# Optimization experiments

Hardware: AMD Instinct MI355X
Metric: run time of the kernel (lower is better)

The kernel has to match this reference:

```python
import jax, jax.numpy as jnp
import numpy as np

N_HEAD = 16


def setup_inputs() -> dict:
    key = jax.random.key(0)
    ks = jax.random.split(key, 5)
    B, T, C = 2, 2048, 1024
    s = 1.0 / np.sqrt(C)
    inp = {
        "x": jax.random.normal(ks[0], (B, T, C), dtype=jnp.float32),
        "Wq": jax.random.normal(ks[1], (C, C), dtype=jnp.float32) * s,
        "bq": jnp.zeros((C,), dtype=jnp.float32),
        "Wk": jax.random.normal(ks[2], (C, C), dtype=jnp.float32) * s,
        "bk": jnp.zeros((C,), dtype=jnp.float32),
        "Wv": jax.random.normal(ks[3], (C, C), dtype=jnp.float32) * s,
        "bv": jnp.zeros((C,), dtype=jnp.float32),
        "Wp": jax.random.normal(ks[4], (C, C), dtype=jnp.float32) * s,
        "bp": jnp.zeros((C,), dtype=jnp.float32),
    }
    return inp


def reference(x, Wq, bq, Wk, bk, Wv, bv, Wp, bp):
    B, T, C = x.shape
    H = N_HEAD
    D = C // H
    # linear projections (torch Linear: x @ W.T + b)
    q = (x @ Wq.T + bq).reshape(B, T, H, D)
    k = (x @ Wk.T + bk).reshape(B, T, H, D)
    v = (x @ Wv.T + bv).reshape(B, T, H, D)
    # scaled dot-product attention (NO causal mask in original forward)
    att = jnp.einsum("bthd,bshd->bhts", q, k) * (1.0 / np.sqrt(D))
    att = jax.nn.softmax(att, axis=-1)
    y = jnp.einsum("bhts,bshd->bthd", att, v).reshape(B, T, C)
    # output projection (dropouts are identity at p=0 / eval)
    return y @ Wp.T + bp
```

## Files before the change

kernel.cpp:

```cpp
#include <hip/hip_runtime.h>
#include <hip/hip_bf16.h>

typedef __attribute__((ext_vector_type(4))) float f32x4;
typedef __attribute__((ext_vector_type(16))) float f32x16;
typedef __attribute__((ext_vector_type(8))) short bf16x8;
typedef __attribute__((ext_vector_type(2))) unsigned int u32x2;

#define T_SEQ 2048
#define C_DIM 1024
#define NH 16
#define DHD 64

__device__ __forceinline__ unsigned cvtpk_bf16(float lo, float hi) {
    unsigned r;
    asm("v_cvt_pk_bf16_f32 %0, %1, %2" : "=v"(r) : "v"(lo), "v"(hi));
    return r;
}

__device__ __forceinline__ float exp2_hw(float x) {
    float r;
    asm("v_exp_f32 %0, %1" : "=v"(r) : "v"(x));
    return r;
}

__device__ __forceinline__ void async_copy16(void* lds, const void* g) {
    __builtin_amdgcn_global_load_lds(
        (const __attribute__((address_space(1))) unsigned int*)(uintptr_t)g,
        (__attribute__((address_space(3))) unsigned int*)(unsigned int)(uintptr_t)lds,
        16, 0, 0);
}

__global__ __launch_bounds__(256) void cvt_all(const float* __restrict__ x,
                                               const float* __restrict__ Wq, const float* __restrict__ Wk,
                                               const float* __restrict__ Wv, const float* __restrict__ Wp,
                                               __hip_bfloat16* __restrict__ xb,
                                               __hip_bfloat16* __restrict__ wf,
                                               __hip_bfloat16* __restrict__ wpb) {
    int i = blockIdx.x * blockDim.x + threadIdx.x;
    const float* src; __hip_bfloat16* dst; int off;
    if (i < 1048576) { src = x; dst = xb; off = i; }
    else {
        int j = i - 1048576; int wi = j >> 18; off = j & 262143;
        switch (wi) {
            case 0:  src = Wq; dst = wf;           break;
            case 1:  src = Wk; dst = wf + 1048576; break;
            case 2:  src = Wv; dst = wf + 2097152; break;
            default: src = Wp; dst = wpb;          break;
        }
    }
    float4 v = *(const float4*)(src + (size_t)off * 4);
    union { __hip_bfloat16 h[4]; u32x2 u; } p;
    p.h[0] = __float2bfloat16(v.x); p.h[1] = __float2bfloat16(v.y);
    p.h[2] = __float2bfloat16(v.z); p.h[3] = __float2bfloat16(v.w);
    *(u32x2*)(dst + (size_t)off * 4) = p.u;
}

__global__ __launch_bounds__(512) void gemm_qkv(const __hip_bfloat16* __restrict__ A,
                                                const __hip_bfloat16* __restrict__ Bw,
                                                const float* __restrict__ biasq,
                                                const float* __restrict__ biask,
                                                const float* __restrict__ biasv,
                                                __hip_bfloat16* __restrict__ oq,
                                                __hip_bfloat16* __restrict__ okk,
                                                __hip_bfloat16* __restrict__ ovt) {
    __shared__ __align__(16) char lds[131072];

    const int wg = ((int)blockIdx.x & 7) * 32 + ((int)blockIdx.x >> 3);
    const int m0 = (wg & 31) * 128;
    const int n0 = (wg >> 5) * 384;

    const int tid = threadIdx.x;
    const int w = tid >> 6, l = tid & 63;
    const int wr = w >> 2, wc = w & 3;
    const int lg = l >> 4, lr = l & 15;

    const int sr0 = tid >> 3;
    const int sc0 = (tid & 7) * 16;
    const int gc0 = sc0 ^ ((sr0 & 7) << 4);
    const size_t goff = (size_t)sr0 * 2048 + gc0;

    const char* Ag = (const char*)A + (size_t)m0 * 2048;
    const char* Bg = (const char*)Bw + (size_t)n0 * 2048;

    auto STAGE_A = [&](int buf, int half, int kt) {
        const char* g = Ag + (size_t)(half * 64) * 2048 + kt * 128 + goff;
        char* d = lds + (buf * 2 + half) * 8192 + w * 1024;
        async_copy16(d, g);
    };
    auto STAGE_B = [&](int buf, int half, int kt) {
        #pragma unroll
        for (int p = 0; p < 3; p++) {
            const char* g = Bg + (size_t)(half * 192 + p * 64) * 2048 + kt * 128 + goff;
            char* d = lds + 32768 + (buf * 2 + half) * 24576 + p * 8192 + w * 1024;
            async_copy16(d, g);
        }
    };

    const int sw = (lr & 7) << 4;
    auto LDA = [&](bf16x8* af, int buf) {
        const char* base = lds + (buf * 2 + wr) * 8192;
        #pragma unroll
        for (int m = 0; m < 4; m++) {
            const int r = m * 16 + lr;
            #pragma unroll
            for (int kk = 0; kk < 2; kk++)
                af[m * 2 + kk] = *(const bf16x8*)(base + r * 128 + ((kk * 64 + lg * 16) ^ sw));
        }
    };
    auto LDB = [&](bf16x8* bfv, int buf, int nq) {
        const char* base = lds + 32768 + (buf * 2 + (wc >> 1)) * 24576;
        #pragma unroll
        for (int n = 0; n < 2; n++) {
            const int r = (wc & 1) * 96 + (nq * 2 + n) * 16 + lr;
            #pragma unroll
            for (int kk = 0; kk < 2; kk++)
                bfv[n * 2 + kk] = *(const bf16x8*)(base + r * 128 + ((kk * 64 + lg * 16) ^ sw));
        }
    };

    f32x4 acc[4][6] = {};
    auto MF = [&](const bf16x8* af, const bf16x8* bfv, int nq) {
        #pragma unroll
        for (int m = 0; m < 4; m++)
            #pragma unroll
            for (int n = 0; n < 2; n++)
                #pragma unroll
                for (int kk = 0; kk < 2; kk++)
                    acc[m][nq * 2 + n] = __builtin_amdgcn_mfma_f32_16x16x32_bf16(
                        af[m * 2 + kk], bfv[n * 2 + kk], acc[m][nq * 2 + n], 0, 0, 0);
    };

#define PH_OPEN()  __builtin_amdgcn_sched_barrier(0); \
                   __builtin_amdgcn_s_barrier(); \
                   asm volatile("s_waitcnt lgkmcnt(0)" ::: "memory"); \
                   __builtin_amdgcn_sched_barrier(0); \
                   __builtin_amdgcn_s_setprio(1);
#define PH_CLOSE() __builtin_amdgcn_s_setprio(0); \
                   __builtin_amdgcn_sched_barrier(0); \
                   __builtin_amdgcn_s_barrier();
#define PH_CLOSE_VM2() __builtin_amdgcn_s_setprio(0); \
                   asm volatile("s_waitcnt vmcnt(2)" ::: "memory"); \
                   __builtin_amdgcn_sched_barrier(0); \
                   __builtin_amdgcn_s_barrier();
#define PH_CLOSE_VM5() __builtin_amdgcn_s_setprio(0); \
                   asm volatile("s_waitcnt vmcnt(5)" ::: "memory"); \
                   __builtin_amdgcn_sched_barrier(0); \
                   __builtin_amdgcn_s_barrier();

    bf16x8 af[8], bfA[4], bfB[4], bfC[4];

    STAGE_B(0, 0, 0); STAGE_B(0, 1, 0); STAGE_A(0, 0, 0); STAGE_A(0, 1, 0);
    STAGE_A(1, 0, 1); STAGE_A(1, 1, 1); STAGE_B(1, 0, 1);
    asm volatile("s_waitcnt vmcnt(5)" ::: "memory");
    __builtin_amdgcn_sched_barrier(0);
    __builtin_amdgcn_s_barrier();

    for (int it = 0; it < 8; ++it) {
        const int t1 = 2 * it + 1;
        const int c2 = (2 * it + 2 < 16) ? 2 * it + 2 : 14;
        const int c3 = (2 * it + 3 < 16) ? 2 * it + 3 : 15;
        const int b2 = c2 & 1, b3 = c3 & 1;

        LDA(af, 0); LDB(bfA, 0, 0);
        STAGE_B(1, 1, t1);
        PH_OPEN(); MF(af, bfA, 0); PH_CLOSE();
        LDB(bfB, 0, 1);
        STAGE_A(b2, 0, c2); STAGE_A(b2, 1, c2);
        PH_OPEN(); MF(af, bfB, 1); PH_CLOSE();
        LDB(bfC, 0, 2);
        PH_OPEN(); MF(af, bfC, 2); PH_CLOSE_VM2();

        LDA(af, 1); LDB(bfA, 1, 0);
        STAGE_B(b2, 0, c2);
        PH_OPEN(); MF(af, bfA, 0); PH_CLOSE();
        LDB(bfB, 1, 1);
        STAGE_B(b2, 1, c2); STAGE_A(b3, 0, c3); STAGE_A(b3, 1, c3);
        PH_OPEN(); MF(af, bfB, 1); PH_CLOSE();
        LDB(bfC, 1, 2);
        STAGE_B(b3, 0, c3);
        PH_OPEN(); MF(af, bfC, 2); PH_CLOSE_VM5();
    }
#undef PH_OPEN
#undef PH_CLOSE
#undef PH_CLOSE_VM2
#undef PH_CLOSE_VM5

    #pragma unroll
    for (int m = 0; m < 4; m++) {
        const int rowb = m0 + wr * 64 + m * 16 + lg * 4;
        const int b = rowb >> 11, t0r = rowb & 2047;
        #pragma unroll
        for (int nf = 0; nf < 6; nf++) {
            const int col = n0 + wc * 96 + nf * 16 + lr;
            const int proj = col >> 10;
            const int colL = col & 1023;
            const int hh = colL >> 6, dd = colL & 63;
            if (proj < 2) {
                const float* bias = (proj == 0) ? biasq : biask;
                const float bsc = (proj == 0) ? 0.125f * 1.4426950408889634f : 1.0f;
                __hip_bfloat16* dst = (proj == 0) ? oq : okk;
                #pragma unroll
                for (int rr = 0; rr < 4; rr++) {
                    const int row = rowb + rr;
                    float val = (acc[m][nf][rr] + bias[colL]) * bsc;
                    dst[(((size_t)(b * NH + hh)) * T_SEQ + (row & 2047)) * DHD + dd] = __float2bfloat16(val);
                }
            } else {
                const float bv = biasv[colL];
                union { __hip_bfloat16 h[4]; u32x2 u; } p;
                #pragma unroll
                for (int rr = 0; rr < 4; rr++)
                    p.h[rr] = __float2bfloat16(acc[m][nf][rr] + bv);
                *(u32x2*)&ovt[(((size_t)(b * NH + hh)) * DHD + dd) * T_SEQ + t0r] = p.u;
            }
        }
    }
}

__global__ __launch_bounds__(256) void gemm_proj(const __hip_bfloat16* __restrict__ A,
                                                 const __hip_bfloat16* __restrict__ Bw,
                                                 const float* __restrict__ biasp,
                                                 float* __restrict__ outf) {
    __shared__ __align__(16) char As[128 * 128];
    __shared__ __align__(16) char Bs[128 * 128];

    const int nwg = gridDim.x;
    const int cpx = nwg >> 3;
    const int wg = ((int)blockIdx.x & 7) * cpx + ((int)blockIdx.x >> 3);
    const int m0 = (wg & 31) * 128;
    const int n0 = (wg >> 5) * 128;

    const int tid = threadIdx.x;
    const int w = tid >> 6, l = tid & 63;
    const int wr = w >> 1, wc = w & 1;
    const int lg = l >> 4, lr = l & 15;

    const char* Ag = (const char*)A + (size_t)m0 * 2048;
    const char* Bg = (const char*)Bw + (size_t)n0 * 2048;
    const int lrow = l >> 3;
    const int scol = (l & 7) * 16;

    f32x4 acc[4][4] = {};

    for (int kt = 0; kt < 16; ++kt) {
        __syncthreads();
        #pragma unroll
        for (int i = 0; i < 4; i++) {
            const int rb = w * 32 + i * 8;
            const size_t go = (size_t)(rb + lrow) * 2048 + (size_t)kt * 128 + scol;
            async_copy16(&As[rb * 128], Ag + go);
            async_copy16(&Bs[rb * 128], Bg + go);
        }
        __syncthreads();
        #pragma unroll
        for (int kk = 0; kk < 2; kk++) {
            bf16x8 af[4], bfr[4];
            #pragma unroll
            for (int m = 0; m < 4; m++)
                af[m] = *(const bf16x8*)(&As[(wr * 64 + m * 16 + lr) * 128 + kk * 64 + lg * 16]);
            #pragma unroll
            for (int n = 0; n < 4; n++)
                bfr[n] = *(const bf16x8*)(&Bs[(wc * 64 + n * 16 + lr) * 128 + kk * 64 + lg * 16]);
            #pragma unroll
            for (int m = 0; m < 4; m++)
                #pragma unroll
                for (int n = 0; n < 4; n++)
                    acc[m][n] = __builtin_amdgcn_mfma_f32_16x16x32_bf16(af[m], bfr[n], acc[m][n], 0, 0, 0);
        }
    }

    #pragma unroll
    for (int m = 0; m < 4; m++)
        #pragma unroll
        for (int n = 0; n < 4; n++)
            #pragma unroll
            for (int r = 0; r < 4; r++) {
                int row = m0 + wr * 64 + m * 16 + lg * 4 + r;
                int col = n0 + wc * 64 + n * 16 + lr;
                outf[(size_t)row * C_DIM + col] = acc[m][n][r] + biasp[col];
            }
}

__global__ __launch_bounds__(256) void attn8(const __hip_bfloat16* __restrict__ Q,
                                             const __hip_bfloat16* __restrict__ K,
                                             const __hip_bfloat16* __restrict__ Vt,
                                             __hip_bfloat16* __restrict__ Y) {
    const int bid = blockIdx.x;
    const int xcd = bid & 7, slot = bid >> 3;
    const int head = xcd * 4 + (slot & 3);
    const int qblk = slot >> 2;

    const int tid = threadIdx.x;
    const int w = tid >> 6, l = tid & 63;
    const int lq = l & 31, hi = l >> 5;
    const int q0 = qblk * 128 + w * 32;

    __shared__ __align__(16) char Ks[3][8192];
    __shared__ __align__(16) char Vs[3][8192];
    __shared__ float bc[4][32];

    const char* Kb = (const char*)(K + (size_t)head * T_SEQ * DHD);
    const char* Vb = (const char*)(Vt + (size_t)head * DHD * T_SEQ);

    bf16x8 qf[4];
    {
        const char* qrow = (const char*)(Q + ((size_t)head * T_SEQ + q0 + lq) * DHD);
        #pragma unroll
        for (int t = 0; t < 4; t++) qf[t] = *(const bf16x8*)(qrow + t * 32 + hi * 16);
    }

    f32x16 yacc[2] = {};
    float ls0 = 0.f, ls1 = 0.f, ls2 = 0.f, ls3 = 0.f;

    const int o0 = (2 * w) * 1024 + l * 16;
    const int o1 = o0 + 1024;
    const int r0 = o0 >> 7, c0b = o0 & 127;
    const int r1 = o1 >> 7, c1b = o1 & 127;
    const int wads0 = r0 * 128 + (c0b ^ ((r0 & 7) << 4));
    const int wads1 = r1 * 128 + (c1b ^ ((r1 & 7) << 4));
    const char* vsrc0 = Vb + (size_t)r0 * (T_SEQ * 2) + c0b;
    const char* vsrc1 = Vb + (size_t)r1 * (T_SEQ * 2) + c1b;

    float4 kreg0, kreg1, vreg0, vreg1;
    auto stage_load = [&](int tile) {
        const char* kb2 = Kb + (size_t)tile * 8192;
        kreg0 = *(const float4*)(kb2 + o0);
        kreg1 = *(const float4*)(kb2 + o1);
        vreg0 = *(const float4*)(vsrc0 + (size_t)tile * 128);
        vreg1 = *(const float4*)(vsrc1 + (size_t)tile * 128);
    };
    auto stage_write = [&](int buf) {
        *(float4*)(&Ks[buf][wads0]) = kreg0;
        *(float4*)(&Ks[buf][wads1]) = kreg1;
        *(float4*)(&Vs[buf][wads0]) = vreg0;
        *(float4*)(&Vs[buf][wads1]) = vreg1;
    };

    auto qk = [&](int buf, f32x16& s0h, f32x16& s1h) {
        s0h = f32x16{}; s1h = f32x16{};
        const char* base0 = Ks[buf] + lq * 128;
        const char* base1 = Ks[buf] + (32 + lq) * 128;
        const int sw0 = (lq & 7) << 4;
        __builtin_amdgcn_s_setprio(1);
        #pragma unroll
        for (int t = 0; t < 4; t++) {
            bf16x8 kf0 = *(const bf16x8*)(base0 + ((t * 32 + hi * 16) ^ sw0));
            s0h = __builtin_amdgcn_mfma_f32_32x32x16_bf16(kf0, qf[t], s0h, 0, 0, 0);
        }
        #pragma unroll
        for (int t = 0; t < 4; t++) {
            bf16x8 kf1 = *(const bf16x8*)(base1 + ((t * 32 + hi * 16) ^ sw0));
            s1h = __builtin_amdgcn_mfma_f32_32x32x16_bf16(kf1, qf[t], s1h, 0, 0, 0);
        }
        __builtin_amdgcn_s_setprio(0);
    };

    auto sm_exp = [&](f32x16& a, f32x16& b) {
        #pragma unroll
        for (int r = 0; r < 16; r += 4) {
            a[r + 0] = exp2_hw(a[r + 0]); a[r + 1] = exp2_hw(a[r + 1]);
            a[r + 2] = exp2_hw(a[r + 2]); a[r + 3] = exp2_hw(a[r + 3]);
            b[r + 0] = exp2_hw(b[r + 0]); b[r + 1] = exp2_hw(b[r + 1]);
            b[r + 2] = exp2_hw(b[r + 2]); b[r + 3] = exp2_hw(b[r + 3]);
            ls0 += a[r + 0] + b[r + 0];
            ls1 += a[r + 1] + b[r + 1];
            ls2 += a[r + 2] + b[r + 2];
            ls3 += a[r + 3] + b[r + 3];
        }
    };

    auto pv = [&](int buf, const f32x16& a, const f32x16& b) {
        unsigned pw0[8], pw1[8];
        #pragma unroll
        for (int M = 0; M < 4; M++) {
            const int u = M * 4;
            pw0[M] = cvtpk_bf16(a[u + 0], a[u + 1]);
            pw1[M] = cvtpk_bf16(a[u + 2], a[u + 3]);
            pw0[M + 4] = cvtpk_bf16(b[u + 0], b[u + 1]);
            pw1[M + 4] = cvtpk_bf16(b[u + 2], b[u + 3]);
        }
        __builtin_amdgcn_s_setprio(1);
        #pragma unroll
        for (int t = 0; t < 4; t++) {
            u32x2 s0p = __builtin_amdgcn_permlane32_swap(pw0[2 * t], pw0[2 * t + 1], false, false);
            u32x2 s1p = __builtin_amdgcn_permlane32_swap(pw1[2 * t], pw1[2 * t + 1], false, false);
            union { unsigned u[4]; bf16x8 v; } af;
            af.u[0] = s0p.x; af.u[1] = s1p.x; af.u[2] = s0p.y; af.u[3] = s1p.y;
            #pragma unroll
            for (int dh = 0; dh < 2; dh++) {
                const int row = dh * 32 + lq;
                bf16x8 vf = *(const bf16x8*)(&Vs[buf][row * 128 + ((t * 32 + hi * 16) ^ ((row & 7) << 4))]);
                yacc[dh] = __builtin_amdgcn_mfma_f32_32x32x16_bf16(af.v, vf, yacc[dh], 0, 0, 0);
            }
        }
        __builtin_amdgcn_s_setprio(0);
    };

    f32x16 sA0, sA1, sB0, sB1;
    stage_load(0); stage_write(0);
    stage_load(1); stage_write(1);
    stage_load(2);
    __syncthreads();
    qk(0, sA0, sA1);

    for (int t = 0; t < 32; t += 2) {
        qk((t + 1) % 3, sB0, sB1);
        if (t + 2 < 32) {
            asm volatile("s_waitcnt vmcnt(0)" ::: "memory");
            stage_write((t + 2) % 3);
            if (t + 3 < 32) stage_load(t + 3);
        }
        sm_exp(sA0, sA1);
        pv(t % 3, sA0, sA1);
        asm volatile("s_waitcnt lgkmcnt(0)" ::: "memory");
        __builtin_amdgcn_s_barrier();
        __builtin_amdgcn_sched_barrier(0);

        const int t1 = t + 1;
        if (t1 + 1 < 32) qk((t1 + 1) % 3, sA0, sA1);
        if (t1 + 2 < 32) {
            asm volatile("s_waitcnt vmcnt(0)" ::: "memory");
            stage_write((t1 + 2) % 3);
            if (t1 + 3 < 32) stage_load(t1 + 3);
        }
        sm_exp(sB0, sB1);
        pv(t1 % 3, sB0, sB1);
        asm volatile("s_waitcnt lgkmcnt(0)" ::: "memory");
        __builtin_amdgcn_s_barrier();
        __builtin_amdgcn_sched_barrier(0);
    }

    float lsum = (ls0 + ls1) + (ls2 + ls3);
    lsum += __shfl_xor(lsum, 32);
    float inv = 1.0f / lsum;
    if (hi == 0) bc[w][lq] = inv;
    asm volatile("s_waitcnt lgkmcnt(0)" ::: "memory");
    __builtin_amdgcn_sched_barrier(0);

    const int b = head >> 4, h16 = head & 15;
    const size_t rowbase = (size_t)b * T_SEQ + q0;
    #pragma unroll
    for (int r = 0; r < 16; r++) {
        const int crow = (r & 3) + 8 * (r >> 2) + 4 * hi;
        const float iv = bc[w][crow];
        const size_t row = rowbase + crow;
        Y[row * C_DIM + h16 * DHD + lq]      = __float2bfloat16(yacc[0][r] * iv);
        Y[row * C_DIM + h16 * DHD + 32 + lq] = __float2bfloat16(yacc[1][r] * iv);
    }
}

extern "C" void kernel_launch(void* const* d_in, const int* in_sizes, int n_in,
                              void* d_out, int out_size, void* d_ws, size_t ws_size,
                              hipStream_t stream) {
    (void)in_sizes; (void)n_in; (void)out_size; (void)ws_size;
    const float* x  = (const float*)d_in[0];
    const float* Wq = (const float*)d_in[1];
    const float* bq = (const float*)d_in[2];
    const float* Wk = (const float*)d_in[3];
    const float* bk = (const float*)d_in[4];
    const float* Wv = (const float*)d_in[5];
    const float* bv = (const float*)d_in[6];
    const float* Wp = (const float*)d_in[7];
    const float* bp = (const float*)d_in[8];
    float* out = (float*)d_out;

    char* ws = (char*)d_ws;
    const size_t MC = (size_t)4096 * C_DIM;
    const size_t CC = (size_t)C_DIM * C_DIM;
    __hip_bfloat16* xb  = (__hip_bfloat16*)ws;  ws += MC * 2;
    __hip_bfloat16* wf  = (__hip_bfloat16*)ws;  ws += 3 * CC * 2;
    __hip_bfloat16* wpb = (__hip_bfloat16*)ws;  ws += CC * 2;
    __hip_bfloat16* qb  = (__hip_bfloat16*)ws;  ws += MC * 2;
    __hip_bfloat16* kb  = (__hip_bfloat16*)ws;  ws += MC * 2;
    __hip_bfloat16* vtb = (__hip_bfloat16*)ws;  ws += MC * 2;
    __hip_bfloat16* yb  = (__hip_bfloat16*)ws;  ws += MC * 2;

    cvt_all<<<8192, 256, 0, stream>>>(x, Wq, Wk, Wv, Wp, xb, wf, wpb);

    gemm_qkv<<<256, 512, 0, stream>>>(xb, wf, bq, bk, bv, qb, kb, vtb);

    attn8<<<512, 256, 0, stream>>>(qb, kb, vtb, yb);

    gemm_proj<<<256, 256, 0, stream>>>(yb, wpb, bp, out);
}
```

Baseline: 119.2 us.

## Process 64 query rows per wave in attention to reuse K/V fragments

Each attention wave now computes two 32-row query tiles against every K/V tile loaded into shared memory, doubling MFMA work per LDS fragment read and halving the grid to 256 blocks. The two-stage ping-pong of score tiles is replaced by a simple single-tile loop with a rotating triple buffer. This cuts LDS traffic and global K/V reloads per query, at the cost of more registers, fewer resident waves and less overlap between QK, softmax and PV phases.

Result: slower. 123.4 us (+3.5%).

```diff
diff --git a/kernel.cpp b/kernel.cpp
--- a/kernel.cpp
+++ b/kernel.cpp
@@ -281,10 +281,10 @@
             }
 }
 
-__global__ __launch_bounds__(256) void attn8(const __hip_bfloat16* __restrict__ Q,
-                                             const __hip_bfloat16* __restrict__ K,
-                                             const __hip_bfloat16* __restrict__ Vt,
-                                             __hip_bfloat16* __restrict__ Y) {
+__global__ __launch_bounds__(256) void attn10(const __hip_bfloat16* __restrict__ Q,
+                                              const __hip_bfloat16* __restrict__ K,
+                                              const __hip_bfloat16* __restrict__ Vt,
+                                              __hip_bfloat16* __restrict__ Y) {
     const int bid = blockIdx.x;
     const int xcd = bid & 7, slot = bid >> 3;
     const int head = xcd * 4 + (slot & 3);
@@ -293,24 +293,29 @@
     const int tid = threadIdx.x;
     const int w = tid >> 6, l = tid & 63;
     const int lq = l & 31, hi = l >> 5;
-    const int q0 = qblk * 128 + w * 32;
+    const int q0 = qblk * 256 + w * 64;
 
     __shared__ __align__(16) char Ks[3][8192];
     __shared__ __align__(16) char Vs[3][8192];
-    __shared__ float bc[4][32];
+    __shared__ float bc[4][64];
 
     const char* Kb = (const char*)(K + (size_t)head * T_SEQ * DHD);
     const char* Vb = (const char*)(Vt + (size_t)head * DHD * T_SEQ);
 
-    bf16x8 qf[4];
+    bf16x8 qfA[4], qfB[4];
     {
-        const char* qrow = (const char*)(Q + ((size_t)head * T_SEQ + q0 + lq) * DHD);
-        #pragma unroll
-        for (int t = 0; t < 4; t++) qf[t] = *(const bf16x8*)(qrow + t * 32 + hi * 16);
-    }
-
-    f32x16 yacc[2] = {};
-    float ls0 = 0.f, ls1 = 0.f, ls2 = 0.f, ls3 = 0.f;
+        const char* qrowA = (const char*)(Q + ((size_t)head * T_SEQ + q0 + lq) * DHD);
+        const char* qrowB = qrowA + 32 * DHD * 2;
+        #pragma unroll
+        for (int t = 0; t < 4; t++) {
+            qfA[t] = *(const bf16x8*)(qrowA + t * 32 + hi * 16);
+            qfB[t] = *(const bf16x8*)(qrowB + t * 32 + hi * 16);
+        }
+    }
+
+    f32x16 yacc[4] = {};
+    float lsA0 = 0.f, lsA1 = 0.f, lsA2 = 0.f, lsA3 = 0.f;
+    float lsB0 = 0.f, lsB1 = 0.f, lsB2 = 0.f, lsB3 = 0.f;
 
     const int o0 = (2 * w) * 1024 + l * 16;
     const int o1 = o0 + 1024;
@@ -336,8 +341,10 @@
         *(float4*)(&Vs[buf][wads1]) = vreg1;
     };
 
-    auto qk = [&](int buf, f32x16& s0h, f32x16& s1h) {
-        s0h = f32x16{}; s1h = f32x16{};
+    f32x16 sA0, sA1, sC0, sC1;
+
+    auto qk = [&](int buf) {
+        sA0 = f32x16{}; sA1 = f32x16{}; sC0 = f32x16{}; sC1 = f32x16{};
         const char* base0 = Ks[buf] + lq * 128;
         const char* base1 = Ks[buf] + (32 + lq) * 128;
         const int sw0 = (lq & 7) << 4;
@@ -345,107 +352,109 @@
         #pragma unroll
         for (int t = 0; t < 4; t++) {
             bf16x8 kf0 = *(const bf16x8*)(base0 + ((t * 32 + hi * 16) ^ sw0));
-            s0h = __builtin_amdgcn_mfma_f32_32x32x16_bf16(kf0, qf[t], s0h, 0, 0, 0);
+            sA0 = __builtin_amdgcn_mfma_f32_32x32x16_bf16(kf0, qfA[t], sA0, 0, 0, 0);
+            sC0 = __builtin_amdgcn_mfma_f32_32x32x16_bf16(kf0, qfB[t], sC0, 0, 0, 0);
         }
         #pragma unroll
         for (int t = 0; t < 4; t++) {
             bf16x8 kf1 = *(const bf16x8*)(base1 + ((t * 32 + hi * 16) ^ sw0));
-            s1h = __builtin_amdgcn_mfma_f32_32x32x16_bf16(kf1, qf[t], s1h, 0, 0, 0);
+            sA1 = __builtin_amdgcn_mfma_f32_32x32x16_bf16(kf1, qfA[t], sA1, 0, 0, 0);
+            sC1 = __builtin_amdgcn_mfma_f32_32x32x16_bf16(kf1, qfB[t], sC1, 0, 0, 0);
         }
         __builtin_amdgcn_s_setprio(0);
     };
 
-    auto sm_exp = [&](f32x16& a, f32x16& b) {
+    auto sm_exp = [&]() {
         #pragma unroll
         for (int r = 0; r < 16; r += 4) {
-            a[r + 0] = exp2_hw(a[r + 0]); a[r + 1] = exp2_hw(a[r + 1]);
-            a[r + 2] = exp2_hw(a[r + 2]); a[r + 3] = exp2_hw(a[r + 3]);
-            b[r + 0] = exp2_hw(b[r + 0]); b[r + 1] = exp2_hw(b[r + 1]);
-            b[r + 2] = exp2_hw(b[r + 2]); b[r + 3] = exp2_hw(b[r + 3]);
-            ls0 += a[r + 0] + b[r + 0];
-            ls1 += a[r + 1] + b[r + 1];
-            ls2 += a[r + 2] + b[r + 2];
-            ls3 += a[r + 3] + b[r + 3];
-        }
-    };
-
-    auto pv = [&](int buf, const f32x16& a, const f32x16& b) {
-        unsigned pw0[8], pw1[8];
+            sA0[r+0]=exp2_hw(sA0[r+0]); sA0[r+1]=exp2_hw(sA0[r+1]); sA0[r+2]=exp2_hw(sA0[r+2]); sA0[r+3]=exp2_hw(sA0[r+3]);
+            sA1[r+0]=exp2_hw(sA1[r+0]); sA1[r+1]=exp2_hw(sA1[r+1]); sA1[r+2]=exp2_hw(sA1[r+2]); sA1[r+3]=exp2_hw(sA1[r+3]);
+            sC0[r+0]=exp2_hw(sC0[r+0]); sC0[r+1]=exp2_hw(sC0[r+1]); sC0[r+2]=exp2_hw(sC0[r+2]); sC0[r+3]=exp2_hw(sC0[r+3]);
+            sC1[r+0]=exp2_hw(sC1[r+0]); sC1[r+1]=exp2_hw(sC1[r+1]); sC1[r+2]=exp2_hw(sC1[r+2]); sC1[r+3]=exp2_hw(sC1[r+3]);
+            lsA0 += sA0[r+0] + sA1[r+0];  lsA1 += sA0[r+1] + sA1[r+1];
+            lsA2 += sA0[r+2] + sA1[r+2];  lsA3 += sA0[r+3] + sA1[r+3];
+            lsB0 += sC0[r+0] + sC1[r+0];  lsB1 += sC0[r+1] + sC1[r+1];
+            lsB2 += sC0[r+2] + sC1[r+2];  lsB3 += sC0[r+3] + sC1[r+3];
+        }
+    };
+
+    auto pv = [&](int buf) {
+        unsigned pwA0[8], pwA1[8], pwB0[8], pwB1[8];
         #pragma unroll
         for (int M = 0; M < 4; M++) {
             const int u = M * 4;
-            pw0[M] = cvtpk_bf16(a[u + 0], a[u + 1]);
-            pw1[M] = cvtpk_bf16(a[u + 2], a[u + 3]);
-            pw0[M + 4] = cvtpk_bf16(b[u + 0], b[u + 1]);
-            pw1[M + 4] = cvtpk_bf16(b[u + 2], b[u + 3]);
+            pwA0[M]     = cvtpk_bf16(sA0[u+0], sA0[u+1]);  pwA1[M]     = cvtpk_bf16(sA0[u+2], sA0[u+3]);
+            pwA0[M + 4] = cvtpk_bf16(sA1[u+0], sA1[u+1]);  pwA1[M + 4] = cvtpk_bf16(sA1[u+2], sA1[u+3]);
+            pwB0[M]     = cvtpk_bf16(sC0[u+0], sC0[u+1]);  pwB1[M]     = cvtpk_bf16(sC0[u+2], sC0[u+3]);
+            pwB0[M + 4] = cvtpk_bf16(sC1[u+0], sC1[u+1]);  pwB1[M + 4] = cvtpk_bf16(sC1[u+2], sC1[u+3]);
         }
         __builtin_amdgcn_s_setprio(1);
         #pragma unroll
         for (int t = 0; t < 4; t++) {
-            u32x2 s0p = __builtin_amdgcn_permlane32_swap(pw0[2 * t], pw0[2 * t + 1], false, false);
-            u32x2 s1p = __builtin_amdgcn_permlane32_swap(pw1[2 * t], pw1[2 * t + 1], false, false);
-            union { unsigned u[4]; bf16x8 v; } af;
-            af.u[0] = s0p.x; af.u[1] = s1p.x; af.u[2] = s0p.y; af.u[3] = s1p.y;
+            u32x2 a0 = __builtin_amdgcn_permlane32_swap(pwA0[2*t], pwA0[2*t+1], false, false);
+            u32x2 a1 = __builtin_amdgcn_permlane32_swap(pwA1[2*t], pwA1[2*t+1], false, false);
+            u32x2 b0 = __builtin_amdgcn_permlane32_swap(pwB0[2*t], pwB0[2*t+1], false, false);
+            u32x2 b1 = __builtin_amdgcn_permlane32_swap(pwB1[2*t], pwB1[2*t+1], false, false);
+            union { unsigned u[4]; bf16x8 v; } afA, afB;
+            afA.u[0] = a0.x; afA.u[1] = a1.x; afA.u[2] = a0.y; afA.u[3] = a1.y;
+            afB.u[0] = b0.x; afB.u[1] = b1.x; afB.u[2] = b0.y; afB.u[3] = b1.y;
             #pragma unroll
             for (int dh = 0; dh < 2; dh++) {
                 const int row = dh * 32 + lq;
                 bf16x8 vf = *(const bf16x8*)(&Vs[buf][row * 128 + ((t * 32 + hi * 16) ^ ((row & 7) << 4))]);
-                yacc[dh] = __builtin_amdgcn_mfma_f32_32x32x16_bf16(af.v, vf, yacc[dh], 0, 0, 0);
+                yacc[dh]     = __builtin_amdgcn_mfma_f32_32x32x16_bf16(afA.v, vf, yacc[dh],     0, 0, 0);
+                yacc[2 + dh] = __builtin_amdgcn_mfma_f32_32x32x16_bf16(afB.v, vf, yacc[2 + dh], 0, 0, 0);
             }
         }
         __builtin_amdgcn_s_setprio(0);
     };
 
-    f32x16 sA0, sA1, sB0, sB1;
     stage_load(0); stage_write(0);
     stage_load(1); stage_write(1);
     stage_load(2);
     __syncthreads();
-    qk(0, sA0, sA1);
-
-    for (int t = 0; t < 32; t += 2) {
-        qk((t + 1) % 3, sB0, sB1);
-        if (t + 2 < 32) {
+
+    int buf = 0;
+    for (int t = 0; t < 32; ++t) {
+        qk(buf);
+        if (t < 30) {
             asm volatile("s_waitcnt vmcnt(0)" ::: "memory");
-            stage_write((t + 2) % 3);
-            if (t + 3 < 32) stage_load(t + 3);
-        }
-        sm_exp(sA0, sA1);
-        pv(t % 3, sA0, sA1);
+            int wb = buf + 2; if (wb >= 3) wb -= 3;
+            stage_write(wb);
+            if (t < 29) stage_load(t + 3);
+        }
+        sm_exp();
+        pv(buf);
         asm volatile("s_waitcnt lgkmcnt(0)" ::: "memory");
         __builtin_amdgcn_s_barrier();
         __builtin_amdgcn_sched_barrier(0);
-
-        const int t1 = t + 1;
-        if (t1 + 1 < 32) qk((t1 + 1) % 3, sA0, sA1);
-        if (t1 + 2 < 32) {
-            asm volatile("s_waitcnt vmcnt(0)" ::: "memory");
-            stage_write((t1 + 2) % 3);
-            if (t1 + 3 < 32) stage_load(t1 + 3);
-        }
-        sm_exp(sB0, sB1);
-        pv(t1 % 3, sB0, sB1);
-        asm volatile("s_waitcnt lgkmcnt(0)" ::: "memory");
-        __builtin_amdgcn_s_barrier();
-        __builtin_amdgcn_sched_barrier(0);
-    }
-
-    float lsum = (ls0 + ls1) + (ls2 + ls3);
-    lsum += __shfl_xor(lsum, 32);
-    float inv = 1.0f / lsum;
-    if (hi == 0) bc[w][lq] = inv;
+        if (++buf == 3) buf = 0;
+    }
+
+    float lsumA = (lsA0 + lsA1) + (lsA2 + lsA3);
+    float lsumB = (lsB0 + lsB1) + (lsB2 + lsB3);
+    lsumA += __shfl_xor(lsumA, 32);
+    lsumB += __shfl_xor(lsumB, 32);
+    if (hi == 0) {
+        bc[w][lq] = 1.0f / lsumA;
+        bc[w][32 + lq] = 1.0f / lsumB;
+    }
     asm volatile("s_waitcnt lgkmcnt(0)" ::: "memory");
     __builtin_amdgcn_sched_barrier(0);
 
     const int b = head >> 4, h16 = head & 15;
-    const size_t rowbase = (size_t)b * T_SEQ + q0;
+    const size_t rowbaseA = (size_t)b * T_SEQ + q0;
     #pragma unroll
     for (int r = 0; r < 16; r++) {
         const int crow = (r & 3) + 8 * (r >> 2) + 4 * hi;
-        const float iv = bc[w][crow];
-        const size_t row = rowbase + crow;
-        Y[row * C_DIM + h16 * DHD + lq]      = __float2bfloat16(yacc[0][r] * iv);
-        Y[row * C_DIM + h16 * DHD + 32 + lq] = __float2bfloat16(yacc[1][r] * iv);
+        const float ivA = bc[w][crow];
+        const float ivB = bc[w][32 + crow];
+        const size_t rowA = rowbaseA + crow;
+        const size_t rowB = rowA + 32;
+        Y[rowA * C_DIM + h16 * DHD + lq]      = __float2bfloat16(yacc[0][r] * ivA);
+        Y[rowA * C_DIM + h16 * DHD + 32 + lq] = __float2bfloat16(yacc[1][r] * ivA);
+        Y[rowB * C_DIM + h16 * DHD + lq]      = __float2bfloat16(yacc[2][r] * ivB);
+        Y[rowB * C_DIM + h16 * DHD + 32 + lq] = __float2bfloat16(yacc[3][r] * ivB);
     }
 }
 
@@ -479,7 +488,7 @@
 
     gemm_qkv<<<256, 512, 0, stream>>>(xb, wf, bq, bk, bv, qb, kb, vtb);
 
-    attn8<<<512, 256, 0, stream>>>(qb, kb, vtb, yb);
+    attn10<<<256, 256, 0, stream>>>(qb, kb, vtb, yb);
 
     gemm_proj<<<256, 256, 0, stream>>>(yb, wpb, bp, out);
 }
```

## Rewrite output projection GEMM with 8-wave double-buffered pipelined schedule

Applied to the files above, without the earlier changes.

Replaces the 4-wave output projection GEMM with a 512-thread version. The new kernel double-buffers A/B tiles in 64KB LDS with an XOR-swizzled layout to avoid bank conflicts. It interleaves async global-to-LDS copies with MFMA phases using sched barriers, setprio and partial vmcnt waits, so that load latency is hidden behind compute. The cost is more LDS per block and a fragile hand-tuned barrier schedule. This GEMM is only one of four kernels, which caps the possible overall gain.

After: 113.0 us, median of 2. 5.3% less time.

```diff
diff --git a/kernel.cpp b/kernel.cpp
--- a/kernel.cpp
+++ b/kernel.cpp
@@ -217,66 +217,122 @@
     }
 }
 
-__global__ __launch_bounds__(256) void gemm_proj(const __hip_bfloat16* __restrict__ A,
-                                                 const __hip_bfloat16* __restrict__ Bw,
-                                                 const float* __restrict__ biasp,
-                                                 float* __restrict__ outf) {
-    __shared__ __align__(16) char As[128 * 128];
-    __shared__ __align__(16) char Bs[128 * 128];
-
-    const int nwg = gridDim.x;
-    const int cpx = nwg >> 3;
-    const int wg = ((int)blockIdx.x & 7) * cpx + ((int)blockIdx.x >> 3);
+__global__ __launch_bounds__(512) void gemm_proj2(const __hip_bfloat16* __restrict__ A,
+                                                  const __hip_bfloat16* __restrict__ Bw,
+                                                  const float* __restrict__ biasp,
+                                                  float* __restrict__ outf) {
+    __shared__ __align__(16) char lds[65536];
+
+    const int wg = ((int)blockIdx.x & 7) * 32 + ((int)blockIdx.x >> 3);
     const int m0 = (wg & 31) * 128;
     const int n0 = (wg >> 5) * 128;
 
     const int tid = threadIdx.x;
     const int w = tid >> 6, l = tid & 63;
-    const int wr = w >> 1, wc = w & 1;
+    const int wr = w >> 2, wc = w & 3;
     const int lg = l >> 4, lr = l & 15;
+
+    const int sr0 = tid >> 3;
+    const int sc0 = (tid & 7) * 16;
+    const int gc0 = sc0 ^ ((sr0 & 7) << 4);
+    const size_t goff = (size_t)sr0 * 2048 + gc0;
 
     const char* Ag = (const char*)A + (size_t)m0 * 2048;
     const char* Bg = (const char*)Bw + (size_t)n0 * 2048;
-    const int lrow = l >> 3;
-    const int scol = (l & 7) * 16;
-
-    f32x4 acc[4][4] = {};
-
-    for (int kt = 0; kt < 16; ++kt) {
-        __syncthreads();
-        #pragma unroll
-        for (int i = 0; i < 4; i++) {
-            const int rb = w * 32 + i * 8;
-            const size_t go = (size_t)(rb + lrow) * 2048 + (size_t)kt * 128 + scol;
-            async_copy16(&As[rb * 128], Ag + go);
-            async_copy16(&Bs[rb * 128], Bg + go);
-        }
-        __syncthreads();
-        #pragma unroll
-        for (int kk = 0; kk < 2; kk++) {
-            bf16x8 af[4], bfr[4];
-            #pragma unroll
-            for (int m = 0; m < 4; m++)
-                af[m] = *(const bf16x8*)(&As[(wr * 64 + m * 16 + lr) * 128 + kk * 64 + lg * 16]);
-            #pragma unroll
-            for (int n = 0; n < 4; n++)
-                bfr[n] = *(const bf16x8*)(&Bs[(wc * 64 + n * 16 + lr) * 128 + kk * 64 + lg * 16]);
-            #pragma unroll
-            for (int m = 0; m < 4; m++)
-                #pragma unroll
-                for (int n = 0; n < 4; n++)
-                    acc[m][n] = __builtin_amdgcn_mfma_f32_16x16x32_bf16(af[m], bfr[n], acc[m][n], 0, 0, 0);
-        }
-    }
+
+    auto STAGE_A = [&](int buf, int half, int kt) {
+        const char* g = Ag + (size_t)(half * 64) * 2048 + kt * 128 + goff;
+        char* d = lds + (buf * 2 + half) * 8192 + w * 1024;
+        async_copy16(d, g);
+    };
+    auto STAGE_B = [&](int buf, int half, int kt) {
+        const char* g = Bg + (size_t)(half * 64) * 2048 + kt * 128 + goff;
+        char* d = lds + 32768 + (buf * 2 + half) * 8192 + w * 1024;
+        async_copy16(d, g);
+    };
+
+    const int sw = (lr & 7) << 4;
+    auto LDA = [&](bf16x8* af, int buf) {
+        const char* base = lds + (buf * 2 + wr) * 8192;
+        #pragma unroll
+        for (int m = 0; m < 4; m++) {
+            const int r = m * 16 + lr;
+            #pragma unroll
+            for (int kk = 0; kk < 2; kk++)
+                af[m * 2 + kk] = *(const bf16x8*)(base + r * 128 + ((kk * 64 + lg * 16) ^ sw));
+        }
+    };
+    auto LDB = [&](bf16x8* bfv, int buf, int n) {
+        const char* base = lds + 32768 + (buf * 2 + (wc >> 1)) * 8192;
+        const int r = (wc & 1) * 32 + n * 16 + lr;
+        #pragma unroll
+        for (int kk = 0; kk < 2; kk++)
+            bfv[kk] = *(const bf16x8*)(base + r * 128 + ((kk * 64 + lg * 16) ^ sw));
+    };
+
+    f32x4 acc[4][2] = {};
+    auto MF = [&](const bf16x8* af, const bf16x8* bfv, int n) {
+        #pragma unroll
+        for (int m = 0; m < 4; m++)
+            #pragma unroll
+            for (int kk = 0; kk < 2; kk++)
+                acc[m][n] = __builtin_amdgcn_mfma_f32_16x16x32_bf16(
+                    af[m * 2 + kk], bfv[kk], acc[m][n], 0, 0, 0);
+    };
+
+#define PH_OPEN()  __builtin_amdgcn_sched_barrier(0); \
+                   __builtin_amdgcn_s_barrier(); \
+                   asm volatile("s_waitcnt lgkmcnt(0)" ::: "memory"); \
+                   __builtin_amdgcn_sched_barrier(0); \
+                   __builtin_amdgcn_s_setprio(1);
+#define PH_CLOSE() __builtin_amdgcn_s_setprio(0); \
+                   __builtin_amdgcn_sched_barrier(0); \
+                   __builtin_amdgcn_s_barrier();
+#define PH_CLOSE_VM2() __builtin_amdgcn_s_setprio(0); \
+                   asm volatile("s_waitcnt vmcnt(2)" ::: "memory"); \
+                   __builtin_amdgcn_sched_barrier(0); \
+                   __builtin_amdgcn_s_barrier();
+
+    bf16x8 af[8], bf0[2], bf1[2];
+
+    STAGE_B(0, 0, 0); STAGE_B(0, 1, 0); STAGE_A(0, 0, 0); STAGE_A(0, 1, 0);
+    STAGE_A(1, 0, 1); STAGE_A(1, 1, 1);
+    asm volatile("s_waitcnt vmcnt(2)" ::: "memory");
+    __builtin_amdgcn_sched_barrier(0);
+    __builtin_amdgcn_s_barrier();
+
+    for (int it = 0; it < 8; ++it) {
+        const int t1 = 2 * it + 1;
+        const int c2 = (2 * it + 2 < 16) ? 2 * it + 2 : 14;
+        const int c3 = (2 * it + 3 < 16) ? 2 * it + 3 : 15;
+        const int b2 = c2 & 1, b3 = c3 & 1;
+
+        LDA(af, 0); LDB(bf0, 0, 0);
+        STAGE_B(1, 0, t1); STAGE_B(1, 1, t1);
+        PH_OPEN(); MF(af, bf0, 0); PH_CLOSE();
+        LDB(bf1, 0, 1);
+        STAGE_A(b2, 0, c2); STAGE_A(b2, 1, c2);
+        PH_OPEN(); MF(af, bf1, 1); PH_CLOSE_VM2();
+
+        LDA(af, 1); LDB(bf0, 1, 0);
+        STAGE_B(b2, 0, c2); STAGE_B(b2, 1, c2);
+        PH_OPEN(); MF(af, bf0, 0); PH_CLOSE();
+        LDB(bf1, 1, 1);
+        STAGE_A(b3, 0, c3); STAGE_A(b3, 1, c3);
+        PH_OPEN(); MF(af, bf1, 1); PH_CLOSE_VM2();
+    }
+#undef PH_OPEN
+#undef PH_CLOSE
+#undef PH_CLOSE_VM2
 
     #pragma unroll
     for (int m = 0; m < 4; m++)
         #pragma unroll
-        for (int n = 0; n < 4; n++)
+        for (int n = 0; n < 2; n++)
             #pragma unroll
             for (int r = 0; r < 4; r++) {
                 int row = m0 + wr * 64 + m * 16 + lg * 4 + r;
-                int col = n0 + wc * 64 + n * 16 + lr;
+                int col = n0 + wc * 32 + n * 16 + lr;
                 outf[(size_t)row * C_DIM + col] = acc[m][n][r] + biasp[col];
             }
 }
@@ -481,5 +537,5 @@
 
     attn8<<<512, 256, 0, stream>>>(qb, kb, vtb, yb);
 
-    gemm_proj<<<256, 256, 0, stream>>>(yb, wpb, bp, out);
-}
+    gemm_proj2<<<256, 512, 0, stream>>>(yb, wpb, bp, out);
+}
```
